# Kernel tuning notes

Hardware: AMD Instinct MI355X
Metric: run time of the kernel (lower is better)

## Reference

```python
import jax, jax.numpy as jnp
import numpy as np

B_J0 = 0.01   # baseline threshold
DT = 1.0
BETA = 1.8    # adaptation strength
LENS = 0.5
SCALE = 6.0
HIGHT = 0.15
GAMMA = 0.5


def _gauss(x, mu, sigma):
    return jnp.exp(-(x - mu) ** 2 / (2.0 * sigma ** 2)) / jnp.sqrt(2.0 * jnp.pi) / sigma


@jax.custom_vjp
def spike_fn(x):
    return (x > 0).astype(x.dtype)


def _spike_fwd(x):
    return spike_fn(x), x


def _spike_bwd(x, g):
    # multi-gaussian surrogate gradient (config.gradient_type == 'MG')
    temp = (_gauss(x, 0.0, LENS) * (1.0 + HIGHT)
            - _gauss(x, LENS, SCALE * LENS) * HIGHT
            - _gauss(x, -LENS, SCALE * LENS) * HIGHT)
    return (g * temp * GAMMA,)


spike_fn.defvjp(_spike_fwd, _spike_bwd)


def setup_inputs() -> dict:
    key = jax.random.key(0)
    ks = jax.random.split(key, 20)
    Bt, T, I, H, O = 256, 250, 700, 128, 20
    f32 = jnp.float32
    return {
        'x': jax.random.uniform(ks[0], (Bt, T, I), dtype=f32),
        'mask': jnp.ones((2, H, H), dtype=f32),
        'w_ih1': (jax.random.normal(ks[1], (I, H), dtype=f32) / np.sqrt(I).astype(np.float32)),
        'b_ih1': jnp.zeros((H,), f32),
        'w_h1h1': (jax.random.normal(ks[2], (H, H), dtype=f32) / np.sqrt(H).astype(np.float32)),
        'b_h1h1': jnp.zeros((H,), f32),
        'w_h1h2': (jax.random.normal(ks[3], (H, H), dtype=f32) / np.sqrt(H).astype(np.float32)),
        'b_h1h2': jnp.zeros((H,), f32),
        'w_h2h2': (jax.random.normal(ks[4], (H, H), dtype=f32) / np.sqrt(H).astype(np.float32)),
        'b_h2h2': jnp.zeros((H,), f32),
        'w_h2o': (jax.random.normal(ks[5], (H, O), dtype=f32) / np.sqrt(H).astype(np.float32)),
        'b_h2o': jnp.zeros((O,), f32),
        'tau_adp_h1': 150.0 + 10.0 * jax.random.normal(ks[6], (H,), dtype=f32),
        'tau_adp_h2': 150.0 + 10.0 * jax.random.normal(ks[7], (H,), dtype=f32),
        'tau_m_h1': 20.0 + 5.0 * jax.random.normal(ks[8], (H,), dtype=f32),
        'tau_m_h2': 20.0 + 5.0 * jax.random.normal(ks[9], (H,), dtype=f32),
        'tau_m_o': 20.0 + 5.0 * jax.random.normal(ks[10], (O,), dtype=f32),
        'hid1_mem0': jax.random.uniform(ks[11], (Bt, H), dtype=f32),
        'hid2_mem0': jax.random.uniform(ks[12], (Bt, H), dtype=f32),
        'out_mem0': jax.random.uniform(ks[13], (Bt, O), dtype=f32),
    }


def _forward(x, mask, w_ih1, b_ih1, w_h1h1, b_h1h1, w_h1h2, b_h1h2,
             w_h2h2, b_h2h2, w_h2o, b_h2o, tau_adp_h1, tau_adp_h2,
             tau_m_h1, tau_m_h2, tau_m_o, hid1_mem0, hid2_mem0, out_mem0):
    Bt, T, _ = x.shape
    H = w_ih1.shape[1]
    O = w_h2o.shape[1]
    # dropout mask applied to recurrent weights (weights stored [in, out])
    w11 = w_h1h1 * mask[0]
    w22 = w_h2h2 * mask[1]
    a1 = jnp.exp(-DT / tau_m_h1)
    r1 = jnp.exp(-DT / tau_adp_h1)
    a2 = jnp.exp(-DT / tau_m_h2)
    r2 = jnp.exp(-DT / tau_adp_h2)
    ao = jnp.exp(-DT / tau_m_o)
    # precompute input projection for all timesteps: [T, B, H]
    xin = jnp.einsum('bti,ih->tbh', x, w_ih1) + b_ih1

    def step(carry, inps):
        h1m, h1s, h2m, h2s, om, b1, b2, acc, s1, s2 = carry
        xt, t = inps
        # layer 1 (adaptive LIF)
        i1 = xt + h1s @ w11 + b_h1h1
        b1 = r1 * b1 + (1.0 - r1) * h1s
        B1 = B_J0 + BETA * b1
        h1m = h1m * a1 + (1.0 - a1) * i1 - B1 * h1s * DT
        h1s = spike_fn(h1m - B1)
        s1 = s1 + h1s
        # layer 2 (adaptive LIF)
        i2 = h1s @ w_h1h2 + b_h1h2 + h2s @ w22 + b_h2h2
        b2 = r2 * b2 + (1.0 - r2) * h2s
        B2 = B_J0 + BETA * b2
        h2m = h2m * a2 + (1.0 - a2) * i2 - B2 * h2s * DT
        h2s = spike_fn(h2m - B2)
        s2 = s2 + h2s
        # leaky-integrator readout (no spike)
        io = h2s @ w_h2o + b_h2o
        om = om * ao + (1.0 - ao) * io
        acc = acc + jnp.where(t > 10, jax.nn.softmax(om, axis=-1), 0.0)
        return (h1m, h1s, h2m, h2s, om, b1, b2, acc, s1, s2), None

    zH = jnp.zeros((Bt, H), x.dtype)
    carry0 = (hid1_mem0, zH, hid2_mem0, zH, out_mem0,
              jnp.full((Bt, H), B_J0, x.dtype), jnp.full((Bt, H), B_J0, x.dtype),
              jnp.zeros((Bt, O), x.dtype), zH, zH)
    carry, _ = jax.lax.scan(step, carry0, (xin, jnp.arange(T)))
    output, s1, s2 = carry[7], carry[8], carry[9]
    A_norm = jnp.sum(jnp.abs(w11)) + jnp.sum(jnp.abs(w22))
    return output, s1 / T, s2 / T, A_norm


def reference(x, mask, w_ih1, b_ih1, w_h1h1, b_h1h1, w_h1h2, b_h1h2,
              w_h2h2, b_h2h2, w_h2o, b_h2o, tau_adp_h1, tau_adp_h2,
              tau_m_h1, tau_m_h2, tau_m_o, hid1_mem0, hid2_mem0, out_mem0):
    return _forward(x, mask, w_ih1, b_ih1, w_h1h1, b_h1h1, w_h1h2, b_h1h2,
                    w_h2h2, b_h2h2, w_h2o, b_h2o, tau_adp_h1, tau_adp_h2,
                    tau_m_h1, tau_m_h2, tau_m_o, hid1_mem0, hid2_mem0, out_mem0)
```

## Files before the change

### kernel.cpp

```cpp
#include <hip/hip_runtime.h>
#include <math.h>

#define TT 250
#define BT 256
#define HN 128
#define ON 20
#define KIN 700
#define NKT 22

#define XIN_OFF 0
#define WPKH_OFF 8192000
#define WPKL_OFF 8237056

typedef __attribute__((ext_vector_type(8))) short bf16x8;
typedef __attribute__((ext_vector_type(4))) float f32x4;

__device__ __forceinline__ unsigned short bf16rne(float f) {
    unsigned u = __float_as_uint(f);
    unsigned r = u + 0x7fffu + ((u >> 16) & 1u);
    return (unsigned short)(r >> 16);
}
__device__ __forceinline__ void hilo(float v, short& h, short& l) {
    unsigned short hh = bf16rne(v);
    float vh = __uint_as_float((unsigned)hh << 16);
    h = (short)hh;
    l = (short)bf16rne(v - vh);
}

__device__ __forceinline__ void gl_lds16(const void* g, void* l) {
    __builtin_amdgcn_global_load_lds(
        (const __attribute__((address_space(1))) unsigned int*)g,
        (__attribute__((address_space(3))) unsigned int*)l, 16, 0, 0);
}

__global__ __launch_bounds__(256) void packw(const float* __restrict__ w,
                                             unsigned short* __restrict__ ph,
                                             unsigned short* __restrict__ pl) {
    int i = blockIdx.x * 256 + threadIdx.x;
    int k = i >> 7, c = i & 127;
    float v = (k < KIN) ? w[k * HN + c] : 0.f;
    short h, l;
    hilo(v, h, l);
    int dst = (((k >> 5) * 8 + (c >> 4)) * 64 + (((k >> 3) & 3) * 16 + (c & 15))) * 8 + (k & 7);
    ph[dst] = (unsigned short)h;
    pl[dst] = (unsigned short)l;
}

__global__ __launch_bounds__(512, 2) void gemm_in(const float* __restrict__ x,
        const unsigned short* __restrict__ wph, const unsigned short* __restrict__ wpl,
        const float* __restrict__ bias1, const float* __restrict__ bias2,
        float* __restrict__ xin) {
    __shared__ __align__(16) unsigned char wbuf[2][16384];
    __shared__ __align__(16) unsigned char xbuf[2][16384];
    const int tid = threadIdx.x;
    const int w = tid >> 6, lane = tid & 63;
    const int q = lane >> 4, li = lane & 15;
    const long mbase = (long)blockIdx.x * 128;

    const int xrow1 = tid >> 3;
    const int xrow2 = xrow1 + 64;
    const int xcs1 = (tid & 7) ^ (xrow1 & 7);
    const int xcs2 = (tid & 7) ^ (xrow2 & 7);
    const int wbase = w * 1024;

    f32x4 acc[8];
#pragma unroll
    for (int nt = 0; nt < 8; nt++) acc[nt] = (f32x4){0.f, 0.f, 0.f, 0.f};

    auto stage = [&](int kt, int buf) {
        char* wb = (char*)wbuf[buf];
        char* xb = (char*)xbuf[buf];
        gl_lds16((const char*)wph + kt * 8192 + tid * 16, wb + wbase);
        gl_lds16((const char*)wpl + kt * 8192 + tid * 16, wb + 8192 + wbase);
        int c1 = xcs1, c2 = xcs2;
        if (kt == NKT - 1) {
            if (c1 == 7) c1 = 6;
            if (c2 == 7) c2 = 6;
        }
        gl_lds16((const char*)x + (mbase + xrow1) * (KIN * 4) + kt * 128 + c1 * 16,
                 xb + wbase);
        gl_lds16((const char*)x + (mbase + xrow2) * (KIN * 4) + kt * 128 + c2 * 16,
                 xb + 8192 + wbase);
    };

    stage(0, 0);
    __syncthreads();

    const int xaddr = (w * 16 + li) * 128 + ((q * 32) ^ ((li & 7) << 4));

    for (int kt = 0; kt < NKT; kt++) {
        if (kt + 1 < NKT) stage(kt + 1, (kt + 1) & 1);

        const char* xc = (const char*)xbuf[kt & 1];
        float av[8];
        *(float4*)&av[0] = *(const float4*)(xc + xaddr);
        *(float4*)&av[4] = *(const float4*)(xc + (xaddr ^ 16));

        bf16x8 ah, al;
#pragma unroll
        for (int j = 0; j < 8; j++) {
            short h, l;
            hilo(av[j], h, l);
            ah[j] = h; al[j] = l;
        }

        const bf16x8* cv = (const bf16x8*)&wbuf[kt & 1][0];
#pragma unroll
        for (int nt = 0; nt < 8; nt++) {
            bf16x8 bh = cv[nt * 64 + lane];
            bf16x8 bl = cv[512 + nt * 64 + lane];
            acc[nt] = __builtin_amdgcn_mfma_f32_16x16x32_bf16(ah, bh, acc[nt], 0, 0, 0);
            acc[nt] = __builtin_amdgcn_mfma_f32_16x16x32_bf16(al, bh, acc[nt], 0, 0, 0);
            acc[nt] = __builtin_amdgcn_mfma_f32_16x16x32_bf16(ah, bl, acc[nt], 0, 0, 0);
        }
        __syncthreads();
    }

    float b12[8];
#pragma unroll
    for (int nt = 0; nt < 8; nt++) {
        int c = nt * 16 + li;
        b12[nt] = bias1[c] + bias2[c];
    }
#pragma unroll
    for (int r = 0; r < 4; r++) {
        long m = mbase + w * 16 + q * 4 + r;
        int bq = (int)(((unsigned long long)m * 67109ull) >> 24);
        int tt = (int)m - bq * 250;
        float* dst = xin + ((size_t)tt * BT + bq) * HN;
#pragma unroll
        for (int nt = 0; nt < 8; nt++) dst[nt * 16 + li] = acc[nt][r] + b12[nt];
    }
}

__global__ __launch_bounds__(512, 2) void snn_scan(
    const float* __restrict__ xin, const float* __restrict__ mask,
    const float* __restrict__ w_h1h1, const float* __restrict__ w_h1h2,
    const float* __restrict__ b_h1h2, const float* __restrict__ w_h2h2,
    const float* __restrict__ b_h2h2, const float* __restrict__ w_h2o,
    const float* __restrict__ b_h2o, const float* __restrict__ tau_adp1,
    const float* __restrict__ tau_adp2, const float* __restrict__ taum1,
    const float* __restrict__ taum2, const float* __restrict__ taumo,
    const float* __restrict__ h1m0, const float* __restrict__ h2m0,
    const float* __restrict__ om0, float* __restrict__ out) {

    __shared__ __align__(16) unsigned short sA1[2 * 2048];
    __shared__ __align__(16) unsigned short sA2[2 * 2048];
    __shared__ __align__(16) unsigned short sloW[8 * 3 * 4 * 64 * 8];
    __shared__ __align__(16) unsigned short sloO[2 * 4 * 64 * 8];
    __shared__ float omb[2][16 * ON];
    __shared__ float red[8];

    const int tid = threadIdx.x;
    const int w = tid >> 6, lane = tid & 63;
    const int q = lane >> 4, li = lane & 15;
    const int col = w * 16 + li;
    const int r0 = blockIdx.x * 16;

    bf16x8 h11[4], h22[4], h12[4], hO[4];
    const int ocol = (w == 6) ? li : 16 + li;
    const bool oval = (w >= 6) && (ocol < ON);
    bf16x8* lo11w = (bf16x8*)sloW + w * 768;
    bf16x8* lo22w = lo11w + 256;
    bf16x8* lo12w = lo11w + 512;
    bf16x8* loOw  = (bf16x8*)sloO + ((w >= 6) ? (w - 6) * 256 : 0);
    float pn = 0.f;
#pragma unroll
    for (int kt = 0; kt < 4; kt++) {
        bf16x8 L11, L22, L12, LO;
#pragma unroll
        for (int j = 0; j < 8; j++) {
            const int k = kt * 32 + q * 8 + j;
            const int idx = k * HN + col;
            float v11 = w_h1h1[idx] * mask[idx];
            float v22 = w_h2h2[idx] * mask[HN * HN + idx];
            float v12 = w_h1h2[idx];
            pn += fabsf(v11) + fabsf(v22);
            short hh, ll;
            hilo(v11, hh, ll); h11[kt][j] = hh; L11[j] = ll;
            hilo(v22, hh, ll); h22[kt][j] = hh; L22[j] = ll;
            hilo(v12, hh, ll); h12[kt][j] = hh; L12[j] = ll;
            float vO = oval ? w_h2o[k * ON + ocol] : 0.f;
            hilo(vO, hh, ll); hO[kt][j] = hh; LO[j] = ll;
        }
        lo11w[kt * 64 + lane] = L11;
        lo22w[kt * 64 + lane] = L22;
        lo12w[kt * 64 + lane] = L12;
        if (w >= 6) loOw[kt * 64 + lane] = LO;
    }

    const float a1 = expf(-1.f / taum1[col]);
    const float r1 = expf(-1.f / tau_adp1[col]);
    const float a2 = expf(-1.f / taum2[col]);
    const float r2 = expf(-1.f / tau_adp2[col]);
    const float cc2 = b_h1h2[col] + b_h2h2[col];
    float h1m[4], h2m[4], b1[4], b2[4], c1[4], c2n[4];
    unsigned s1bits = 0, s2bits = 0;
#pragma unroll
    for (int r = 0; r < 4; r++) {
        h1m[r] = h1m0[(r0 + q * 4 + r) * HN + col];
        h2m[r] = h2m0[(r0 + q * 4 + r) * HN + col];
        b1[r] = 0.01f; b2[r] = 0.01f; c1[r] = 0.f; c2n[r] = 0.f;
    }
    const float ao = oval ? expf(-1.f / taumo[ocol]) : 0.f;
    const float bo = oval ? b_h2o[ocol] : 0.f;
    float om[4];
#pragma unroll
    for (int r = 0; r < 4; r++)
        om[r] = oval ? om0[(r0 + q * 4 + r) * ON + ocol] : 0.f;
    const int sm = lane >> 2, ob = (lane & 3) * 5;
    float accs[5] = {0.f, 0.f, 0.f, 0.f, 0.f};

    {
        unsigned* z1 = (unsigned*)sA1;
        unsigned* z2 = (unsigned*)sA2;
        z1[tid] = 0u; z1[tid + 512] = 0u; z1[tid + 1024] = 0u; z1[tid + 1536] = 0u;
        z2[tid] = 0u; z2[tid + 512] = 0u; z2[tid + 1024] = 0u; z2[tid + 1536] = 0u;
    }

#pragma unroll
    for (int off = 32; off > 0; off >>= 1) pn += __shfl_down(pn, off);
    if (lane == 0) red[w] = pn;
    __syncthreads();
    if (tid == 0 && blockIdx.x == 0) {
        float s = 0.f;
#pragma unroll
        for (int i = 0; i < 8; i++) s += red[i];
        out[70656] = s;
    }

    const int wbase = (w >> 1) * 512 + (((2 * w + (li >> 3)) & 3) * 16 + q * 4) * 8 + (li & 7);
    const unsigned short ONE = 0x3F80u;

    const bf16x8* lo11r = (const bf16x8*)sloW + w * 768;
    const bf16x8* lo22r = lo11r + 256;
    const bf16x8* lo12r = lo11r + 512;
    const bf16x8* loOr  = (const bf16x8*)sloO + ((w >= 6) ? (w - 6) * 256 : 0);

    const float* xp = xin + (size_t)(r0 + q * 4) * HN + col;

    for (int i = 0; i < TT; i++) {
        const int pa = i & 1;

        float xt[4];
#pragma unroll
        for (int r = 0; r < 4; r++) xt[r] = xp[r * HN];
        xp += BT * HN;

        const bf16x8* g1p = (const bf16x8*)(sA1 + ((pa ^ 1) << 11));
        const bf16x8* f2p = (const bf16x8*)(sA2 + (pa << 11));
        bf16x8 g1[4], f2[4];
#pragma unroll
        for (int kt = 0; kt < 4; kt++) {
            g1[kt] = g1p[kt * 64 + lane];
            f2[kt] = f2p[kt * 64 + lane];
        }

        f32x4 aJ = {0.f, 0.f, 0.f, 0.f}, aG = {0.f, 0.f, 0.f, 0.f};
        {
            bf16x8 t12[4], t22[4];
#pragma unroll
            for (int kt = 0; kt < 4; kt++) {
                t12[kt] = lo12r[kt * 64 + lane];
                t22[kt] = lo22r[kt * 64 + lane];
            }
#pragma unroll
            for (int kt = 0; kt < 4; kt++) {
                aJ = __builtin_amdgcn_mfma_f32_16x16x32_bf16(g1[kt], h12[kt], aJ, 0, 0, 0);
                aJ = __builtin_amdgcn_mfma_f32_16x16x32_bf16(g1[kt], t12[kt], aJ, 0, 0, 0);
                aG = __builtin_amdgcn_mfma_f32_16x16x32_bf16(f2[kt], h22[kt], aG, 0, 0, 0);
                aG = __builtin_amdgcn_mfma_f32_16x16x32_bf16(f2[kt], t22[kt], aG, 0, 0, 0);
            }
        }
        f32x4 aO = {0.f, 0.f, 0.f, 0.f};
        if (w >= 6) {
            bf16x8 tO[4];
#pragma unroll
            for (int kt = 0; kt < 4; kt++) tO[kt] = loOr[kt * 64 + lane];
#pragma unroll
            for (int kt = 0; kt < 4; kt++) {
                aO = __builtin_amdgcn_mfma_f32_16x16x32_bf16(f2[kt], hO[kt], aO, 0, 0, 0);
                aO = __builtin_amdgcn_mfma_f32_16x16x32_bf16(f2[kt], tO[kt], aO, 0, 0, 0);
            }
        }
        f32x4 aI = {0.f, 0.f, 0.f, 0.f};
        {
            bf16x8 t11[4];
#pragma unroll
            for (int kt = 0; kt < 4; kt++) t11[kt] = lo11r[kt * 64 + lane];
#pragma unroll
            for (int kt = 0; kt < 4; kt++) {
                aI = __builtin_amdgcn_mfma_f32_16x16x32_bf16(g1[kt], h11[kt], aI, 0, 0, 0);
                aI = __builtin_amdgcn_mfma_f32_16x16x32_bf16(g1[kt], t11[kt], aI, 0, 0, 0);
            }
        }

        if (i >= 1) {
            unsigned short* s2w = sA2 + ((pa ^ 1) << 11);
#pragma unroll
            for (int r = 0; r < 4; r++) {
                const float sv = (float)((s2bits >> r) & 1u);
                const float i2 = aJ[r] + aG[r] + cc2;
                b2[r] = r2 * b2[r] + (1.f - r2) * sv;
                const float B = 0.01f + 1.8f * b2[r];
                h2m[r] = a2 * h2m[r] + (1.f - a2) * i2 - B * sv;
                const bool sp = (h2m[r] - B) > 0.f;
                s2bits = sp ? (s2bits | (1u << r)) : (s2bits & ~(1u << r));
                c2n[r] += sp ? 1.f : 0.f;
                s2w[wbase + r * 8] = sp ? ONE : (unsigned short)0;
            }
        }

        if (w >= 6 && i >= 2) {
#pragma unroll
            for (int r = 0; r < 4; r++) {
                om[r] = ao * om[r] + (1.f - ao) * (bo + aO[r]);
                if (oval) omb[pa][(q * 4 + r) * ON + ocol] = om[r];
            }
        }

        if (w == 0 && i >= 14) {
            float v[5], e[5];
            float mx = -1e30f;
#pragma unroll
            for (int s = 0; s < 5; s++) { v[s] = omb[pa ^ 1][sm * ON + ob + s]; mx = fmaxf(mx, v[s]); }
            mx = fmaxf(mx, __shfl_xor(mx, 1));
            mx = fmaxf(mx, __shfl_xor(mx, 2));
            float se = 0.f;
#pragma unroll
            for (int s = 0; s < 5; s++) { e[s] = __expf(v[s] - mx); se += e[s]; }
            se += __shfl_xor(se, 1);
            se += __shfl_xor(se, 2);
            const float inv = 1.f / se;
#pragma unroll
            for (int s = 0; s < 5; s++) accs[s] += e[s] * inv;
        }

        {
            unsigned short* s1w = sA1 + (pa << 11);
#pragma unroll
            for (int r = 0; r < 4; r++) {
                const float sv = (float)((s1bits >> r) & 1u);
                const float i1 = xt[r] + aI[r];
                b1[r] = r1 * b1[r] + (1.f - r1) * sv;
                const float B = 0.01f + 1.8f * b1[r];
                h1m[r] = a1 * h1m[r] + (1.f - a1) * i1 - B * sv;
                const bool sp = (h1m[r] - B) > 0.f;
                s1bits = sp ? (s1bits | (1u << r)) : (s1bits & ~(1u << r));
                c1[r] += sp ? 1.f : 0.f;
                s1w[wbase + r * 8] = sp ? ONE : (unsigned short)0;
            }
        }
        __syncthreads();
    }

    {
        const bf16x8* g1p = (const bf16x8*)(sA1 + 2048);
        const bf16x8* f2p = (const bf16x8*)(sA2);
        bf16x8 g1[4], f2[4], t12[4], t22[4];
#pragma unroll
        for (int kt = 0; kt < 4; kt++) {
            g1[kt] = g1p[kt * 64 + lane];
            f2[kt] = f2p[kt * 64 + lane];
            t12[kt] = lo12r[kt * 64 + lane];
            t22[kt] = lo22r[kt * 64 + lane];
        }
        f32x4 aJ = {0.f, 0.f, 0.f, 0.f}, aG = {0.f, 0.f, 0.f, 0.f};
#pragma unroll
        for (int kt = 0; kt < 4; kt++) {
            aJ = __builtin_amdgcn_mfma_f32_16x16x32_bf16(g1[kt], h12[kt], aJ, 0, 0, 0);
            aJ = __builtin_amdgcn_mfma_f32_16x16x32_bf16(g1[kt], t12[kt], aJ, 0, 0, 0);
            aG = __builtin_amdgcn_mfma_f32_16x16x32_bf16(f2[kt], h22[kt], aG, 0, 0, 0);
            aG = __builtin_amdgcn_mfma_f32_16x16x32_bf16(f2[kt], t22[kt], aG, 0, 0, 0);
        }
        f32x4 aO = {0.f, 0.f, 0.f, 0.f};
        if (w >= 6) {
            bf16x8 tO[4];
#pragma unroll
            for (int kt = 0; kt < 4; kt++) tO[kt] = loOr[kt * 64 + lane];
#pragma unroll
            for (int kt = 0; kt < 4; kt++) {
                aO = __builtin_amdgcn_mfma_f32_16x16x32_bf16(f2[kt], hO[kt], aO, 0, 0, 0);
                aO = __builtin_amdgcn_mfma_f32_16x16x32_bf16(f2[kt], tO[kt], aO, 0, 0, 0);
            }
        }
        {
            unsigned short* s2w = sA2 + 2048;
#pragma unroll
            for (int r = 0; r < 4; r++) {
                const float sv = (float)((s2bits >> r) & 1u);
                const float i2 = aJ[r] + aG[r] + cc2;
                b2[r] = r2 * b2[r] + (1.f - r2) * sv;
                const float B = 0.01f + 1.8f * b2[r];
                h2m[r] = a2 * h2m[r] + (1.f - a2) * i2 - B * sv;
                const bool sp = (h2m[r] - B) > 0.f;
                s2bits = sp ? (s2bits | (1u << r)) : (s2bits & ~(1u << r));
                c2n[r] += sp ? 1.f : 0.f;
                s2w[wbase + r * 8] = sp ? ONE : (unsigned short)0;
            }
        }
        if (w >= 6) {
#pragma unroll
            for (int r = 0; r < 4; r++) {
                om[r] = ao * om[r] + (1.f - ao) * (bo + aO[r]);
                if (oval) omb[0][(q * 4 + r) * ON + ocol] = om[r];
            }
        }
        if (w == 0) {
            float v[5], e[5];
            float mx = -1e30f;
#pragma unroll
            for (int s = 0; s < 5; s++) { v[s] = omb[1][sm * ON + ob + s]; mx = fmaxf(mx, v[s]); }
            mx = fmaxf(mx, __shfl_xor(mx, 1));
            mx = fmaxf(mx, __shfl_xor(mx, 2));
            float se = 0.f;
#pragma unroll
            for (int s = 0; s < 5; s++) { e[s] = __expf(v[s] - mx); se += e[s]; }
            se += __shfl_xor(se, 1);
            se += __shfl_xor(se, 2);
            const float inv = 1.f / se;
#pragma unroll
            for (int s = 0; s < 5; s++) accs[s] += e[s] * inv;
        }
        __syncthreads();
    }
    {
        if (w >= 6) {
            const bf16x8* f2p = (const bf16x8*)(sA2 + 2048);
            bf16x8 f2[4], tO[4];
#pragma unroll
            for (int kt = 0; kt < 4; kt++) {
                f2[kt] = f2p[kt * 64 + lane];
                tO[kt] = loOr[kt * 64 + lane];
            }
            f32x4 aO = {0.f, 0.f, 0.f, 0.f};
#pragma unroll
            for (int kt = 0; kt < 4; kt++) {
                aO = __builtin_amdgcn_mfma_f32_16x16x32_bf16(f2[kt], hO[kt], aO, 0, 0, 0);
                aO = __builtin_amdgcn_mfma_f32_16x16x32_bf16(f2[kt], tO[kt], aO, 0, 0, 0);
            }
#pragma unroll
            for (int r = 0; r < 4; r++) {
                om[r] = ao * om[r] + (1.f - ao) * (bo + aO[r]);
                if (oval) omb[1][(q * 4 + r) * ON + ocol] = om[r];
            }
        }
        if (w == 0) {
            float v[5], e[5];
            float mx = -1e30f;
#pragma unroll
            for (int s = 0; s < 5; s++) { v[s] = omb[0][sm * ON + ob + s]; mx = fmaxf(mx, v[s]); }
            mx = fmaxf(mx, __shfl_xor(mx, 1));
            mx = fmaxf(mx, __shfl_xor(mx, 2));
            float se = 0.f;
#pragma unroll
            for (int s = 0; s < 5; s++) { e[s] = __expf(v[s] - mx); se += e[s]; }
            se += __shfl_xor(se, 1);
            se += __shfl_xor(se, 2);
            const float inv = 1.f / se;
#pragma unroll
            for (int s = 0; s < 5; s++) accs[s] += e[s] * inv;
        }
        __syncthreads();
    }
    if (w == 0) {
        float v[5], e[5];
        float mx = -1e30f;
#pragma unroll
        for (int s = 0; s < 5; s++) { v[s] = omb[1][sm * ON + ob + s]; mx = fmaxf(mx, v[s]); }
        mx = fmaxf(mx, __shfl_xor(mx, 1));
        mx = fmaxf(mx, __shfl_xor(mx, 2));
        float se = 0.f;
#pragma unroll
        for (int s = 0; s < 5; s++) { e[s] = __expf(v[s] - mx); se += e[s]; }
        se += __shfl_xor(se, 1);
        se += __shfl_xor(se, 2);
        const float inv = 1.f / se;
#pragma unroll
        for (int s = 0; s < 5; s++) out[(r0 + sm) * ON + ob + s] = accs[s] + e[s] * inv;
    }
#pragma unroll
    for (int r = 0; r < 4; r++) {
        out[5120 + (r0 + q * 4 + r) * HN + col] = c1[r] * (1.f / 250.f);
        out[37888 + (r0 + q * 4 + r) * HN + col] = c2n[r] * (1.f / 250.f);
    }
}

extern "C" void kernel_launch(void* const* d_in, const int* in_sizes, int n_in,
                              void* d_out, int out_size, void* d_ws, size_t ws_size,
                              hipStream_t stream) {
    const float* x        = (const float*)d_in[0];
    const float* mask     = (const float*)d_in[1];
    const float* w_ih1    = (const float*)d_in[2];
    const float* b_ih1    = (const float*)d_in[3];
    const float* w_h1h1   = (const float*)d_in[4];
    const float* b_h1h1   = (const float*)d_in[5];
    const float* w_h1h2   = (const float*)d_in[6];
    const float* b_h1h2   = (const float*)d_in[7];
    const float* w_h2h2   = (const float*)d_in[8];
    const float* b_h2h2   = (const float*)d_in[9];
    const float* w_h2o    = (const float*)d_in[10];
    const float* b_h2o    = (const float*)d_in[11];
    const float* tau_adp1 = (const float*)d_in[12];
    const float* tau_adp2 = (const float*)d_in[13];
    const float* taum1    = (const float*)d_in[14];
    const float* taum2    = (const float*)d_in[15];
    const float* taumo    = (const float*)d_in[16];
    const float* h1m0     = (const float*)d_in[17];
    const float* h2m0     = (const float*)d_in[18];
    const float* om0      = (const float*)d_in[19];
    float* out = (float*)d_out;
    float* ws  = (float*)d_ws;

    float* xin = ws + XIN_OFF;
    unsigned short* wph = (unsigned short*)(ws + WPKH_OFF);
    unsigned short* wpl = (unsigned short*)(ws + WPKL_OFF);

    packw<<<352, 256, 0, stream>>>(w_ih1, wph, wpl);
    gemm_in<<<500, 512, 0, stream>>>(x, wph, wpl, b_ih1, b_h1h1, xin);
    snn_scan<<<16, 512, 0, stream>>>(xin, mask, w_h1h1, w_h1h2, b_h1h2, w_h2h2,
                                     b_h2h2, w_h2o, b_h2o, tau_adp1, tau_adp2,
                                     taum1, taum2, taumo, h1m0, h2m0, om0, out);
}
```

Before: 577.6 us.

## Keep low-part recurrent weights in registers and unroll scan by two

Moves the bf16 low-part weight fragments from LDS into registers and relaxes launch bounds to one block per CU so the extra VGPRs fit. The time loop is unrolled by two with ping-pong x prefetch registers, the MFMA block runs at raised priority, and the barrier becomes a raw LDS waitcnt plus s_barrier. This removes per-step LDS reads of weights and gives more overlap of the next x load. In exchange it lowers occupancy, and the lighter barrier relies on LDS-only synchronisation being sufficient.

```diff
diff --git a/kernel.cpp b/kernel.cpp
--- a/kernel.cpp
+++ b/kernel.cpp
@@ -26,6 +26,10 @@
     h = (short)hh;
     l = (short)bf16rne(v - vh);
 }
+
+#define LBAR() do { asm volatile("s_waitcnt lgkmcnt(0)" ::: "memory"); \
+                    __builtin_amdgcn_s_barrier();                      \
+                    asm volatile("" ::: "memory"); } while (0)
 
 __device__ __forceinline__ void gl_lds16(const void* g, void* l) {
     __builtin_amdgcn_global_load_lds(
@@ -133,7 +137,7 @@
     }
 }
 
-__global__ __launch_bounds__(512, 2) void snn_scan(
+__global__ __launch_bounds__(512, 1) void snn_scan(
     const float* __restrict__ xin, const float* __restrict__ mask,
     const float* __restrict__ w_h1h1, const float* __restrict__ w_h1h2,
     const float* __restrict__ b_h1h2, const float* __restrict__ w_h2h2,
@@ -146,8 +150,6 @@
 
     __shared__ __align__(16) unsigned short sA1[2 * 2048];
     __shared__ __align__(16) unsigned short sA2[2 * 2048];
-    __shared__ __align__(16) unsigned short sloW[8 * 3 * 4 * 64 * 8];
-    __shared__ __align__(16) unsigned short sloO[2 * 4 * 64 * 8];
     __shared__ float omb[2][16 * ON];
     __shared__ float red[8];
 
@@ -157,17 +159,12 @@
     const int col = w * 16 + li;
     const int r0 = blockIdx.x * 16;
 
-    bf16x8 h11[4], h22[4], h12[4], hO[4];
+    bf16x8 h11[4], l11[4], h22[4], l22[4], h12[4], l12[4], hO[4], lO[4];
     const int ocol = (w == 6) ? li : 16 + li;
     const bool oval = (w >= 6) && (ocol < ON);
-    bf16x8* lo11w = (bf16x8*)sloW + w * 768;
-    bf16x8* lo22w = lo11w + 256;
-    bf16x8* lo12w = lo11w + 512;
-    bf16x8* loOw  = (bf16x8*)sloO + ((w >= 6) ? (w - 6) * 256 : 0);
     float pn = 0.f;
 #pragma unroll
     for (int kt = 0; kt < 4; kt++) {
-        bf16x8 L11, L22, L12, LO;
 #pragma unroll
         for (int j = 0; j < 8; j++) {
             const int k = kt * 32 + q * 8 + j;
@@ -177,16 +174,12 @@
             float v12 = w_h1h2[idx];
             pn += fabsf(v11) + fabsf(v22);
             short hh, ll;
-            hilo(v11, hh, ll); h11[kt][j] = hh; L11[j] = ll;
-            hilo(v22, hh, ll); h22[kt][j] = hh; L22[j] = ll;
-            hilo(v12, hh, ll); h12[kt][j] = hh; L12[j] = ll;
+            hilo(v11, hh, ll); h11[kt][j] = hh; l11[kt][j] = ll;
+            hilo(v22, hh, ll); h22[kt][j] = hh; l22[kt][j] = ll;
+            hilo(v12, hh, ll); h12[kt][j] = hh; l12[kt][j] = ll;
             float vO = oval ? w_h2o[k * ON + ocol] : 0.f;
-            hilo(vO, hh, ll); hO[kt][j] = hh; LO[j] = ll;
-        }
-        lo11w[kt * 64 + lane] = L11;
-        lo22w[kt * 64 + lane] = L22;
-        lo12w[kt * 64 + lane] = L12;
-        if (w >= 6) loOw[kt * 64 + lane] = LO;
+            hilo(vO, hh, ll); hO[kt][j] = hh; lO[kt][j] = ll;
+        }
     }
 
     const float a1 = expf(-1.f / taum1[col]);
@@ -232,71 +225,135 @@
     const int wbase = (w >> 1) * 512 + (((2 * w + (li >> 3)) & 3) * 16 + q * 4) * 8 + (li & 7);
     const unsigned short ONE = 0x3F80u;
 
-    const bf16x8* lo11r = (const bf16x8*)sloW + w * 768;
-    const bf16x8* lo22r = lo11r + 256;
-    const bf16x8* lo12r = lo11r + 512;
-    const bf16x8* loOr  = (const bf16x8*)sloO + ((w >= 6) ? (w - 6) * 256 : 0);
-
     const float* xp = xin + (size_t)(r0 + q * 4) * HN + col;
-
-    for (int i = 0; i < TT; i++) {
-        const int pa = i & 1;
-
-        float xt[4];
-#pragma unroll
-        for (int r = 0; r < 4; r++) xt[r] = xp[r * HN];
-        xp += BT * HN;
-
-        const bf16x8* g1p = (const bf16x8*)(sA1 + ((pa ^ 1) << 11));
-        const bf16x8* f2p = (const bf16x8*)(sA2 + (pa << 11));
+    float xtA[4], xtB[4];
+    xtA[0] = xp[0]; xtA[1] = xp[HN]; xtA[2] = xp[2 * HN]; xtA[3] = xp[3 * HN];
+    xp += BT * HN;
+
+#define STEPX(PA, XTC, XTP, IV)                                                   \
+    {                                                                             \
+        const int i_ = (IV);                                                      \
+                       \
+        XTP[0] = xp[0]; XTP[1] = xp[HN]; XTP[2] = xp[2 * HN]; XTP[3] = xp[3 * HN];\
+        xp += BT * HN;                                                            \
+        const bf16x8* g1p_ = (const bf16x8*)(sA1 + (((PA) ^ 1) << 11));           \
+        const bf16x8* f2p_ = (const bf16x8*)(sA2 + ((PA) << 11));                 \
+        bf16x8 g1[4], f2[4];                                                      \
+        _Pragma("unroll")                                                         \
+        for (int kt = 0; kt < 4; kt++) {                                          \
+            g1[kt] = g1p_[kt * 64 + lane];                                        \
+            f2[kt] = f2p_[kt * 64 + lane];                                        \
+        }                                                                         \
+        f32x4 aI = {0.f, 0.f, 0.f, 0.f}, aJ = {0.f, 0.f, 0.f, 0.f},              \
+              aG = {0.f, 0.f, 0.f, 0.f};                                          \
+        __builtin_amdgcn_s_setprio(1);                                            \
+        _Pragma("unroll")                                                         \
+        for (int kt = 0; kt < 4; kt++) {                                          \
+            aI = __builtin_amdgcn_mfma_f32_16x16x32_bf16(g1[kt], h11[kt], aI, 0, 0, 0); \
+            aI = __builtin_amdgcn_mfma_f32_16x16x32_bf16(g1[kt], l11[kt], aI, 0, 0, 0); \
+            aJ = __builtin_amdgcn_mfma_f32_16x16x32_bf16(g1[kt], h12[kt], aJ, 0, 0, 0); \
+            aJ = __builtin_amdgcn_mfma_f32_16x16x32_bf16(g1[kt], l12[kt], aJ, 0, 0, 0); \
+            aG = __builtin_amdgcn_mfma_f32_16x16x32_bf16(f2[kt], h22[kt], aG, 0, 0, 0); \
+            aG = __builtin_amdgcn_mfma_f32_16x16x32_bf16(f2[kt], l22[kt], aG, 0, 0, 0); \
+        }                                                                         \
+        f32x4 aO = {0.f, 0.f, 0.f, 0.f};                                          \
+        if (w >= 6) {                                                             \
+            _Pragma("unroll")                                                     \
+            for (int kt = 0; kt < 4; kt++) {                                      \
+                aO = __builtin_amdgcn_mfma_f32_16x16x32_bf16(f2[kt], hO[kt], aO, 0, 0, 0); \
+                aO = __builtin_amdgcn_mfma_f32_16x16x32_bf16(f2[kt], lO[kt], aO, 0, 0, 0); \
+            }                                                                     \
+        }                                                                         \
+        __builtin_amdgcn_s_setprio(0);                                            \
+        if (i_ >= 1) {                                                            \
+            unsigned short* s2w = sA2 + (((PA) ^ 1) << 11);                       \
+            _Pragma("unroll")                                                     \
+            for (int r = 0; r < 4; r++) {                                         \
+                const float sv = (float)((s2bits >> r) & 1u);                     \
+                const float i2 = aJ[r] + aG[r] + cc2;                             \
+                b2[r] = r2 * b2[r] + (1.f - r2) * sv;                             \
+                const float B = 0.01f + 1.8f * b2[r];                             \
+                h2m[r] = a2 * h2m[r] + (1.f - a2) * i2 - B * sv;                  \
+                const bool sp = (h2m[r] - B) > 0.f;                               \
+                s2bits = sp ? (s2bits | (1u << r)) : (s2bits & ~(1u << r));       \
+                c2n[r] += sp ? 1.f : 0.f;                                         \
+                s2w[wbase + r * 8] = sp ? ONE : (unsigned short)0;                \
+            }                                                                     \
+        }                                                                         \
+        if (w >= 6 && i_ >= 2) {                                                  \
+            _Pragma("unroll")                                                     \
+            for (int r = 0; r < 4; r++) {                                         \
+                om[r] = ao * om[r] + (1.f - ao) * (bo + aO[r]);                   \
+                if (oval) omb[(PA)][(q * 4 + r) * ON + ocol] = om[r];             \
+            }                                                                     \
+        }                                                                         \
+        if (w == 0 && i_ >= 14) {                                                 \
+            float v_[5], e_[5];                                                   \
+            float mx = -1e30f;                                                    \
+            _Pragma("unroll")                                                     \
+            for (int s = 0; s < 5; s++) { v_[s] = omb[(PA) ^ 1][sm * ON + ob + s]; mx = fmaxf(mx, v_[s]); } \
+            mx = fmaxf(mx, __shfl_xor(mx, 1));                                    \
+            mx = fmaxf(mx, __shfl_xor(mx, 2));                                    \
+            float se = 0.f;                                                       \
+            _Pragma("unroll")                                                     \
+            for (int s = 0; s < 5; s++) { e_[s] = __expf(v_[s] - mx); se += e_[s]; } \
+            se += __shfl_xor(se, 1);                                              \
+            se += __shfl_xor(se, 2);                                              \
+            const float inv = 1.f / se;                                           \
+            _Pragma("unroll")                                                     \
+            for (int s = 0; s < 5; s++) accs[s] += e_[s] * inv;                   \
+        }                                                                         \
+        {                                                                         \
+            unsigned short* s1w = sA1 + ((PA) << 11);                             \
+            _Pragma("unroll")                                                     \
+            for (int r = 0; r < 4; r++) {                                         \
+                const float sv = (float)((s1bits >> r) & 1u);                     \
+                const float i1 = XTC[r] + aI[r];                                  \
+                b1[r] = r1 * b1[r] + (1.f - r1) * sv;                             \
+                const float B = 0.01f + 1.8f * b1[r];                             \
+                h1m[r] = a1 * h1m[r] + (1.f - a1) * i1 - B * sv;                  \
+                const bool sp = (h1m[r] - B) > 0.f;                               \
+                s1bits = sp ? (s1bits | (1u << r)) : (s1bits & ~(1u << r));       \
+                c1[r] += sp ? 1.f : 0.f;                                          \
+                s1w[wbase + r * 8] = sp ? ONE : (unsigned short)0;                \
+            }                                                                     \
+        }                                                                         \
+        LBAR();                                                                   \
+    }
+
+    for (int it = 0; it < TT; it += 2) {
+        STEPX(0, xtA, xtB, it);
+        STEPX(1, xtB, xtA, it + 1);
+    }
+#undef STEPX
+
+    {
+        const bf16x8* g1p = (const bf16x8*)(sA1 + 2048);
+        const bf16x8* f2p = (const bf16x8*)(sA2);
         bf16x8 g1[4], f2[4];
 #pragma unroll
         for (int kt = 0; kt < 4; kt++) {
             g1[kt] = g1p[kt * 64 + lane];
             f2[kt] = f2p[kt * 64 + lane];
         }
-
         f32x4 aJ = {0.f, 0.f, 0.f, 0.f}, aG = {0.f, 0.f, 0.f, 0.f};
-        {
-            bf16x8 t12[4], t22[4];
-#pragma unroll
-            for (int kt = 0; kt < 4; kt++) {
-                t12[kt] = lo12r[kt * 64 + lane];
-                t22[kt] = lo22r[kt * 64 + lane];
-            }
-#pragma unroll
-            for (int kt = 0; kt < 4; kt++) {
-                aJ = __builtin_amdgcn_mfma_f32_16x16x32_bf16(g1[kt], h12[kt], aJ, 0, 0, 0);
-                aJ = __builtin_amdgcn_mfma_f32_16x16x32_bf16(g1[kt], t12[kt], aJ, 0, 0, 0);
-                aG = __builtin_amdgcn_mfma_f32_16x16x32_bf16(f2[kt], h22[kt], aG, 0, 0, 0);
-                aG = __builtin_amdgcn_mfma_f32_16x16x32_bf16(f2[kt], t22[kt], aG, 0, 0, 0);
-            }
+#pragma unroll
+        for (int kt = 0; kt < 4; kt++) {
+            aJ = __builtin_amdgcn_mfma_f32_16x16x32_bf16(g1[kt], h12[kt], aJ, 0, 0, 0);
+            aJ = __builtin_amdgcn_mfma_f32_16x16x32_bf16(g1[kt], l12[kt], aJ, 0, 0, 0);
+            aG = __builtin_amdgcn_mfma_f32_16x16x32_bf16(f2[kt], h22[kt], aG, 0, 0, 0);
+            aG = __builtin_amdgcn_mfma_f32_16x16x32_bf16(f2[kt], l22[kt], aG, 0, 0, 0);
         }
         f32x4 aO = {0.f, 0.f, 0.f, 0.f};
         if (w >= 6) {
-            bf16x8 tO[4];
-#pragma unroll
-            for (int kt = 0; kt < 4; kt++) tO[kt] = loOr[kt * 64 + lane];
 #pragma unroll
             for (int kt = 0; kt < 4; kt++) {
                 aO = __builtin_amdgcn_mfma_f32_16x16x32_bf16(f2[kt], hO[kt], aO, 0, 0, 0);
-                aO = __builtin_amdgcn_mfma_f32_16x16x32_bf16(f2[kt], tO[kt], aO, 0, 0, 0);
+                aO = __builtin_amdgcn_mfma_f32_16x16x32_bf16(f2[kt], lO[kt], aO, 0, 0, 0);
             }
         }
-        f32x4 aI = {0.f, 0.f, 0.f, 0.f};
         {
-            bf16x8 t11[4];
-#pragma unroll
-            for (int kt = 0; kt < 4; kt++) t11[kt] = lo11r[kt * 64 + lane];
-#pragma unroll
-            for (int kt = 0; kt < 4; kt++) {
-                aI = __builtin_amdgcn_mfma_f32_16x16x32_bf16(g1[kt], h11[kt], aI, 0, 0, 0);
-                aI = __builtin_amdgcn_mfma_f32_16x16x32_bf16(g1[kt], t11[kt], aI, 0, 0, 0);
-            }
-        }
-
-        if (i >= 1) {
-            unsigned short* s2w = sA2 + ((pa ^ 1) << 11);
+            unsigned short* s2w = sA2 + 2048;
 #pragma unroll
             for (int r = 0; r < 4; r++) {
                 const float sv = (float)((s2bits >> r) & 1u);
@@ -310,20 +367,18 @@
                 s2w[wbase + r * 8] = sp ? ONE : (unsigned short)0;
             }
         }
-
-        if (w >= 6 && i >= 2) {
+        if (w >= 6) {
 #pragma unroll
             for (int r = 0; r < 4; r++) {
                 om[r] = ao * om[r] + (1.f - ao) * (bo + aO[r]);
-                if (oval) omb[pa][(q * 4 + r) * ON + ocol] = om[r];
+                if (oval) omb[0][(q * 4 + r) * ON + ocol] = om[r];
             }
         }
-
-        if (w == 0 && i >= 14) {
+        if (w == 0) {
             float v[5], e[5];
             float mx = -1e30f;
 #pragma unroll
-            for (int s = 0; s < 5; s++) { v[s] = omb[pa ^ 1][sm * ON + ob + s]; mx = fmaxf(mx, v[s]); }
+            for (int s = 0; s < 5; s++) { v[s] = omb[1][sm * ON + ob + s]; mx = fmaxf(mx, v[s]); }
             mx = fmaxf(mx, __shfl_xor(mx, 1));
             mx = fmaxf(mx, __shfl_xor(mx, 2));
             float se = 0.f;
@@ -335,109 +390,19 @@
 #pragma unroll
             for (int s = 0; s < 5; s++) accs[s] += e[s] * inv;
         }
-
-        {
-            unsigned short* s1w = sA1 + (pa << 11);
-#pragma unroll
-            for (int r = 0; r < 4; r++) {
-                const float sv = (float)((s1bits >> r) & 1u);
-                const float i1 = xt[r] + aI[r];
-                b1[r] = r1 * b1[r] + (1.f - r1) * sv;
-                const float B = 0.01f + 1.8f * b1[r];
-                h1m[r] = a1 * h1m[r] + (1.f - a1) * i1 - B * sv;
-                const bool sp = (h1m[r] - B) > 0.f;
-                s1bits = sp ? (s1bits | (1u << r)) : (s1bits & ~(1u << r));
-                c1[r] += sp ? 1.f : 0.f;
-                s1w[wbase + r * 8] = sp ? ONE : (unsigned short)0;
-            }
-        }
-        __syncthreads();
-    }
-
-    {
-        const bf16x8* g1p = (const bf16x8*)(sA1 + 2048);
-        const bf16x8* f2p = (const bf16x8*)(sA2);
-        bf16x8 g1[4], f2[4], t12[4], t22[4];
-#pragma unroll
-        for (int kt = 0; kt < 4; kt++) {
-            g1[kt] = g1p[kt * 64 + lane];
-            f2[kt] = f2p[kt * 64 + lane];
-            t12[kt] = lo12r[kt * 64 + lane];
-            t22[kt] = lo22r[kt * 64 + lane];
-        }
-        f32x4 aJ = {0.f, 0.f, 0.f, 0.f}, aG = {0.f, 0.f, 0.f, 0.f};
-#pragma unroll
-        for (int kt = 0; kt < 4; kt++) {
-            aJ = __builtin_amdgcn_mfma_f32_16x16x32_bf16(g1[kt], h12[kt], aJ, 0, 0, 0);
-            aJ = __builtin_amdgcn_mfma_f32_16x16x32_bf16(g1[kt], t12[kt], aJ, 0, 0, 0);
-            aG = __builtin_amdgcn_mfma_f32_16x16x32_bf16(f2[kt], h22[kt], aG, 0, 0, 0);
-            aG = __builtin_amdgcn_mfma_f32_16x16x32_bf16(f2[kt], t22[kt], aG, 0, 0, 0);
-        }
-        f32x4 aO = {0.f, 0.f, 0.f, 0.f};
-        if (w >= 6) {
-            bf16x8 tO[4];
-#pragma unroll
-            for (int kt = 0; kt < 4; kt++) tO[kt] = loOr[kt * 64 + lane];
-#pragma unroll
-            for (int kt = 0; kt < 4; kt++) {
-                aO = __builtin_amdgcn_mfma_f32_16x16x32_bf16(f2[kt], hO[kt], aO, 0, 0, 0);
-                aO = __builtin_amdgcn_mfma_f32_16x16x32_bf16(f2[kt], tO[kt], aO, 0, 0, 0);
-            }
-        }
-        {
-            unsigned short* s2w = sA2 + 2048;
-#pragma unroll
-            for (int r = 0; r < 4; r++) {
-                const float sv = (float)((s2bits >> r) & 1u);
-                const float i2 = aJ[r] + aG[r] + cc2;
-                b2[r] = r2 * b2[r] + (1.f - r2) * sv;
-                const float B = 0.01f + 1.8f * b2[r];
-                h2m[r] = a2 * h2m[r] + (1.f - a2) * i2 - B * sv;
-                const bool sp = (h2m[r] - B) > 0.f;
-                s2bits = sp ? (s2bits | (1u << r)) : (s2bits & ~(1u << r));
-                c2n[r] += sp ? 1.f : 0.f;
-                s2w[wbase + r * 8] = sp ? ONE : (unsigned short)0;
-            }
-        }
-        if (w >= 6) {
-#pragma unroll
-            for (int r = 0; r < 4; r++) {
-                om[r] = ao * om[r] + (1.f - ao) * (bo + aO[r]);
-                if (oval) omb[0][(q * 4 + r) * ON + ocol] = om[r];
-            }
-        }
-        if (w == 0) {
-            float v[5], e[5];
-            float mx = -1e30f;
-#pragma unroll
-            for (int s = 0; s < 5; s++) { v[s] = omb[1][sm * ON + ob + s]; mx = fmaxf(mx, v[s]); }
-            mx = fmaxf(mx, __shfl_xor(mx, 1));
-            mx = fmaxf(mx, __shfl_xor(mx, 2));
-            float se = 0.f;
-#pragma unroll
-            for (int s = 0; s < 5; s++) { e[s] = __expf(v[s] - mx); se += e[s]; }
-            se += __shfl_xor(se, 1);
-            se += __shfl_xor(se, 2);
-            const float inv = 1.f / se;
-#pragma unroll
-            for (int s = 0; s < 5; s++) accs[s] += e[s] * inv;
-        }
         __syncthreads();
     }
     {
         if (w >= 6) {
             const bf16x8* f2p = (const bf16x8*)(sA2 + 2048);
-            bf16x8 f2[4], tO[4];
-#pragma unroll
-            for (int kt = 0; kt < 4; kt++) {
-                f2[kt] = f2p[kt * 64 + lane];
-                tO[kt] = loOr[kt * 64 + lane];
-            }
+            bf16x8 f2[4];
+#pragma unroll
+            for (int kt = 0; kt < 4; kt++) f2[kt] = f2p[kt * 64 + lane];
             f32x4 aO = {0.f, 0.f, 0.f, 0.f};
 #pragma unroll
             for (int kt = 0; kt < 4; kt++) {
                 aO = __builtin_amdgcn_mfma_f32_16x16x32_bf16(f2[kt], hO[kt], aO, 0, 0, 0);
-                aO = __builtin_amdgcn_mfma_f32_16x16x32_bf16(f2[kt], tO[kt], aO, 0, 0, 0);
+                aO = __builtin_amdgcn_mfma_f32_16x16x32_bf16(f2[kt], lO[kt], aO, 0, 0, 0);
             }
 #pragma unroll
             for (int r = 0; r < 4; r++) {
```

Result: slower. 614.9 us (+6.5%).

## Keep split-bf16 recurrent weights in registers and split readout GEMM across warps

Applied to the files above, without the earlier changes.

The low-order bf16 halves of the recurrent weight matrices now live in registers instead of being reloaded from shared memory every timestep. This removes per-step LDS traffic and frees the large shared buffers. The output projection's hi and lo MFMA halves are split between warps 4-5 (lo part) and warps 6-7 (hi part). The lo partials are exchanged through a small shared buffer, which adds one more pipeline stage and an extra epilogue step. The cost is much higher VGPR pressure under launch_bounds(512,2), which risks spills or lower occupancy.

```diff
diff --git a/kernel.cpp b/kernel.cpp
--- a/kernel.cpp
+++ b/kernel.cpp
@@ -146,8 +146,7 @@
 
     __shared__ __align__(16) unsigned short sA1[2 * 2048];
     __shared__ __align__(16) unsigned short sA2[2 * 2048];
-    __shared__ __align__(16) unsigned short sloW[8 * 3 * 4 * 64 * 8];
-    __shared__ __align__(16) unsigned short sloO[2 * 4 * 64 * 8];
+    __shared__ __align__(16) float oxb[2][512];
     __shared__ float omb[2][16 * ON];
     __shared__ float red[8];
 
@@ -157,17 +156,13 @@
     const int col = w * 16 + li;
     const int r0 = blockIdx.x * 16;
 
-    bf16x8 h11[4], h22[4], h12[4], hO[4];
-    const int ocol = (w == 6) ? li : 16 + li;
-    const bool oval = (w >= 6) && (ocol < ON);
-    bf16x8* lo11w = (bf16x8*)sloW + w * 768;
-    bf16x8* lo22w = lo11w + 256;
-    bf16x8* lo12w = lo11w + 512;
-    bf16x8* loOw  = (bf16x8*)sloO + ((w >= 6) ? (w - 6) * 256 : 0);
+    bf16x8 h11[4], l11[4], h22[4], l22[4], h12[4], l12[4], wO[4];
+    const int ocol = ((w & 1) ? 16 : 0) + li;
+    const bool ow    = (w >= 4) && (ocol < ON);
+    const bool oval6 = (w >= 6) && (ocol < ON);
     float pn = 0.f;
 #pragma unroll
     for (int kt = 0; kt < 4; kt++) {
-        bf16x8 L11, L22, L12, LO;
 #pragma unroll
         for (int j = 0; j < 8; j++) {
             const int k = kt * 32 + q * 8 + j;
@@ -177,16 +172,13 @@
             float v12 = w_h1h2[idx];
             pn += fabsf(v11) + fabsf(v22);
             short hh, ll;
-            hilo(v11, hh, ll); h11[kt][j] = hh; L11[j] = ll;
-            hilo(v22, hh, ll); h22[kt][j] = hh; L22[j] = ll;
-            hilo(v12, hh, ll); h12[kt][j] = hh; L12[j] = ll;
-            float vO = oval ? w_h2o[k * ON + ocol] : 0.f;
-            hilo(vO, hh, ll); hO[kt][j] = hh; LO[j] = ll;
-        }
-        lo11w[kt * 64 + lane] = L11;
-        lo22w[kt * 64 + lane] = L22;
-        lo12w[kt * 64 + lane] = L12;
-        if (w >= 6) loOw[kt * 64 + lane] = LO;
+            hilo(v11, hh, ll); h11[kt][j] = hh; l11[kt][j] = ll;
+            hilo(v22, hh, ll); h22[kt][j] = hh; l22[kt][j] = ll;
+            hilo(v12, hh, ll); h12[kt][j] = hh; l12[kt][j] = ll;
+            float vO = ow ? w_h2o[k * ON + ocol] : 0.f;
+            hilo(vO, hh, ll);
+            wO[kt][j] = (w >= 6) ? hh : ll;
+        }
     }
 
     const float a1 = expf(-1.f / taum1[col]);
@@ -202,14 +194,17 @@
         h2m[r] = h2m0[(r0 + q * 4 + r) * HN + col];
         b1[r] = 0.01f; b2[r] = 0.01f; c1[r] = 0.f; c2n[r] = 0.f;
     }
-    const float ao = oval ? expf(-1.f / taumo[ocol]) : 0.f;
-    const float bo = oval ? b_h2o[ocol] : 0.f;
+    const float ao = oval6 ? expf(-1.f / taumo[ocol]) : 0.f;
+    const float bo = oval6 ? b_h2o[ocol] : 0.f;
     float om[4];
 #pragma unroll
     for (int r = 0; r < 4; r++)
-        om[r] = oval ? om0[(r0 + q * 4 + r) * ON + ocol] : 0.f;
+        om[r] = oval6 ? om0[(r0 + q * 4 + r) * ON + ocol] : 0.f;
     const int sm = lane >> 2, ob = (lane & 3) * 5;
     float accs[5] = {0.f, 0.f, 0.f, 0.f, 0.f};
+
+    f32x4 aOp = {0.f, 0.f, 0.f, 0.f};
+    const int oidx = ((w & 1) << 8) + lane * 4;
 
     {
         unsigned* z1 = (unsigned*)sA1;
@@ -232,11 +227,6 @@
     const int wbase = (w >> 1) * 512 + (((2 * w + (li >> 3)) & 3) * 16 + q * 4) * 8 + (li & 7);
     const unsigned short ONE = 0x3F80u;
 
-    const bf16x8* lo11r = (const bf16x8*)sloW + w * 768;
-    const bf16x8* lo22r = lo11r + 256;
-    const bf16x8* lo12r = lo11r + 512;
-    const bf16x8* loOr  = (const bf16x8*)sloO + ((w >= 6) ? (w - 6) * 256 : 0);
-
     const float* xp = xin + (size_t)(r0 + q * 4) * HN + col;
 
     for (int i = 0; i < TT; i++) {
@@ -256,43 +246,21 @@
             f2[kt] = f2p[kt * 64 + lane];
         }
 
-        f32x4 aJ = {0.f, 0.f, 0.f, 0.f}, aG = {0.f, 0.f, 0.f, 0.f};
-        {
-            bf16x8 t12[4], t22[4];
-#pragma unroll
-            for (int kt = 0; kt < 4; kt++) {
-                t12[kt] = lo12r[kt * 64 + lane];
-                t22[kt] = lo22r[kt * 64 + lane];
-            }
-#pragma unroll
-            for (int kt = 0; kt < 4; kt++) {
-                aJ = __builtin_amdgcn_mfma_f32_16x16x32_bf16(g1[kt], h12[kt], aJ, 0, 0, 0);
-                aJ = __builtin_amdgcn_mfma_f32_16x16x32_bf16(g1[kt], t12[kt], aJ, 0, 0, 0);
-                aG = __builtin_amdgcn_mfma_f32_16x16x32_bf16(f2[kt], h22[kt], aG, 0, 0, 0);
-                aG = __builtin_amdgcn_mfma_f32_16x16x32_bf16(f2[kt], t22[kt], aG, 0, 0, 0);
-            }
+        f32x4 aI = {0.f, 0.f, 0.f, 0.f}, aJ = {0.f, 0.f, 0.f, 0.f}, aG = {0.f, 0.f, 0.f, 0.f};
+#pragma unroll
+        for (int kt = 0; kt < 4; kt++) {
+            aI = __builtin_amdgcn_mfma_f32_16x16x32_bf16(g1[kt], h11[kt], aI, 0, 0, 0);
+            aI = __builtin_amdgcn_mfma_f32_16x16x32_bf16(g1[kt], l11[kt], aI, 0, 0, 0);
+            aJ = __builtin_amdgcn_mfma_f32_16x16x32_bf16(g1[kt], h12[kt], aJ, 0, 0, 0);
+            aJ = __builtin_amdgcn_mfma_f32_16x16x32_bf16(g1[kt], l12[kt], aJ, 0, 0, 0);
+            aG = __builtin_amdgcn_mfma_f32_16x16x32_bf16(f2[kt], h22[kt], aG, 0, 0, 0);
+            aG = __builtin_amdgcn_mfma_f32_16x16x32_bf16(f2[kt], l22[kt], aG, 0, 0, 0);
         }
         f32x4 aO = {0.f, 0.f, 0.f, 0.f};
-        if (w >= 6) {
-            bf16x8 tO[4];
-#pragma unroll
-            for (int kt = 0; kt < 4; kt++) tO[kt] = loOr[kt * 64 + lane];
-#pragma unroll
-            for (int kt = 0; kt < 4; kt++) {
-                aO = __builtin_amdgcn_mfma_f32_16x16x32_bf16(f2[kt], hO[kt], aO, 0, 0, 0);
-                aO = __builtin_amdgcn_mfma_f32_16x16x32_bf16(f2[kt], tO[kt], aO, 0, 0, 0);
-            }
-        }
-        f32x4 aI = {0.f, 0.f, 0.f, 0.f};
-        {
-            bf16x8 t11[4];
-#pragma unroll
-            for (int kt = 0; kt < 4; kt++) t11[kt] = lo11r[kt * 64 + lane];
-#pragma unroll
-            for (int kt = 0; kt < 4; kt++) {
-                aI = __builtin_amdgcn_mfma_f32_16x16x32_bf16(g1[kt], h11[kt], aI, 0, 0, 0);
-                aI = __builtin_amdgcn_mfma_f32_16x16x32_bf16(g1[kt], t11[kt], aI, 0, 0, 0);
-            }
+        if (w >= 4) {
+#pragma unroll
+            for (int kt = 0; kt < 4; kt++)
+                aO = __builtin_amdgcn_mfma_f32_16x16x32_bf16(f2[kt], wO[kt], aO, 0, 0, 0);
         }
 
         if (i >= 1) {
@@ -311,29 +279,35 @@
             }
         }
 
-        if (w >= 6 && i >= 2) {
-#pragma unroll
-            for (int r = 0; r < 4; r++) {
-                om[r] = ao * om[r] + (1.f - ao) * (bo + aO[r]);
-                if (oval) omb[pa][(q * 4 + r) * ON + ocol] = om[r];
-            }
-        }
-
-        if (w == 0 && i >= 14) {
-            float v[5], e[5];
+        if (w >= 4 && w < 6) {
+#pragma unroll
+            for (int r = 0; r < 4; r++) oxb[pa][oidx + r] = aO[r];
+        }
+
+        if (w >= 6 && i >= 3) {
+#pragma unroll
+            for (int r = 0; r < 4; r++) {
+                om[r] = ao * om[r] + (1.f - ao) * (bo + aOp[r] + oxb[pa ^ 1][oidx + r]);
+                if (oval6) omb[pa][(q * 4 + r) * ON + ocol] = om[r];
+            }
+        }
+        aOp = aO;
+
+        if (w == 0 && i >= 15) {
+            float v_[5], e_[5];
             float mx = -1e30f;
 #pragma unroll
-            for (int s = 0; s < 5; s++) { v[s] = omb[pa ^ 1][sm * ON + ob + s]; mx = fmaxf(mx, v[s]); }
+            for (int s = 0; s < 5; s++) { v_[s] = omb[pa ^ 1][sm * ON + ob + s]; mx = fmaxf(mx, v_[s]); }
             mx = fmaxf(mx, __shfl_xor(mx, 1));
             mx = fmaxf(mx, __shfl_xor(mx, 2));
             float se = 0.f;
 #pragma unroll
-            for (int s = 0; s < 5; s++) { e[s] = __expf(v[s] - mx); se += e[s]; }
+            for (int s = 0; s < 5; s++) { e_[s] = __expf(v_[s] - mx); se += e_[s]; }
             se += __shfl_xor(se, 1);
             se += __shfl_xor(se, 2);
             const float inv = 1.f / se;
 #pragma unroll
-            for (int s = 0; s < 5; s++) accs[s] += e[s] * inv;
+            for (int s = 0; s < 5; s++) accs[s] += e_[s] * inv;
         }
 
         {
@@ -357,32 +331,25 @@
     {
         const bf16x8* g1p = (const bf16x8*)(sA1 + 2048);
         const bf16x8* f2p = (const bf16x8*)(sA2);
-        bf16x8 g1[4], f2[4], t12[4], t22[4];
+        bf16x8 g1[4], f2[4];
 #pragma unroll
         for (int kt = 0; kt < 4; kt++) {
             g1[kt] = g1p[kt * 64 + lane];
             f2[kt] = f2p[kt * 64 + lane];
-            t12[kt] = lo12r[kt * 64 + lane];
-            t22[kt] = lo22r[kt * 64 + lane];
         }
         f32x4 aJ = {0.f, 0.f, 0.f, 0.f}, aG = {0.f, 0.f, 0.f, 0.f};
 #pragma unroll
         for (int kt = 0; kt < 4; kt++) {
             aJ = __builtin_amdgcn_mfma_f32_16x16x32_bf16(g1[kt], h12[kt], aJ, 0, 0, 0);
-            aJ = __builtin_amdgcn_mfma_f32_16x16x32_bf16(g1[kt], t12[kt], aJ, 0, 0, 0);
+            aJ = __builtin_amdgcn_mfma_f32_16x16x32_bf16(g1[kt], l12[kt], aJ, 0, 0, 0);
             aG = __builtin_amdgcn_mfma_f32_16x16x32_bf16(f2[kt], h22[kt], aG, 0, 0, 0);
-            aG = __builtin_amdgcn_mfma_f32_16x16x32_bf16(f2[kt], t22[kt], aG, 0, 0, 0);
+            aG = __builtin_amdgcn_mfma_f32_16x16x32_bf16(f2[kt], l22[kt], aG, 0, 0, 0);
         }
         f32x4 aO = {0.f, 0.f, 0.f, 0.f};
-        if (w >= 6) {
-            bf16x8 tO[4];
-#pragma unroll
-            for (int kt = 0; kt < 4; kt++) tO[kt] = loOr[kt * 64 + lane];
-#pragma unroll
-            for (int kt = 0; kt < 4; kt++) {
-                aO = __builtin_amdgcn_mfma_f32_16x16x32_bf16(f2[kt], hO[kt], aO, 0, 0, 0);
-                aO = __builtin_amdgcn_mfma_f32_16x16x32_bf16(f2[kt], tO[kt], aO, 0, 0, 0);
-            }
+        if (w >= 4) {
+#pragma unroll
+            for (int kt = 0; kt < 4; kt++)
+                aO = __builtin_amdgcn_mfma_f32_16x16x32_bf16(f2[kt], wO[kt], aO, 0, 0, 0);
         }
         {
             unsigned short* s2w = sA2 + 2048;
@@ -399,13 +366,18 @@
                 s2w[wbase + r * 8] = sp ? ONE : (unsigned short)0;
             }
         }
+        if (w >= 4 && w < 6) {
+#pragma unroll
+            for (int r = 0; r < 4; r++) oxb[0][oidx + r] = aO[r];
+        }
         if (w >= 6) {
 #pragma unroll
             for (int r = 0; r < 4; r++) {
-                om[r] = ao * om[r] + (1.f - ao) * (bo + aO[r]);
-                if (oval) omb[0][(q * 4 + r) * ON + ocol] = om[r];
-            }
-        }
+                om[r] = ao * om[r] + (1.f - ao) * (bo + aOp[r] + oxb[1][oidx + r]);
+                if (oval6) omb[0][(q * 4 + r) * ON + ocol] = om[r];
+            }
+        }
+        aOp = aO;
         if (w == 0) {
             float v[5], e[5];
             float mx = -1e30f;
@@ -425,26 +397,28 @@
         __syncthreads();
     }
     {
+        f32x4 aO = {0.f, 0.f, 0.f, 0.f};
+        if (w >= 4) {
+            const bf16x8* f2p = (const bf16x8*)(sA2 + 2048);
+            bf16x8 f2[4];
+#pragma unroll
+            for (int kt = 0; kt < 4; kt++) f2[kt] = f2p[kt * 64 + lane];
+#pragma unroll
+            for (int kt = 0; kt < 4; kt++)
+                aO = __builtin_amdgcn_mfma_f32_16x16x32_bf16(f2[kt], wO[kt], aO, 0, 0, 0);
+        }
+        if (w >= 4 && w < 6) {
+#pragma unroll
+            for (int r = 0; r < 4; r++) oxb[1][oidx + r] = aO[r];
+        }
         if (w >= 6) {
-            const bf16x8* f2p = (const bf16x8*)(sA2 + 2048);
-            bf16x8 f2[4], tO[4];
-#pragma unroll
-            for (int kt = 0; kt < 4; kt++) {
-                f2[kt] = f2p[kt * 64 + lane];
-                tO[kt] = loOr[kt * 64 + lane];
-            }
-            f32x4 aO = {0.f, 0.f, 0.f, 0.f};
-#pragma unroll
-            for (int kt = 0; kt < 4; kt++) {
-                aO = __builtin_amdgcn_mfma_f32_16x16x32_bf16(f2[kt], hO[kt], aO, 0, 0, 0);
-                aO = __builtin_amdgcn_mfma_f32_16x16x32_bf16(f2[kt], tO[kt], aO, 0, 0, 0);
-            }
-#pragma unroll
-            for (int r = 0; r < 4; r++) {
-                om[r] = ao * om[r] + (1.f - ao) * (bo + aO[r]);
-                if (oval) omb[1][(q * 4 + r) * ON + ocol] = om[r];
-            }
-        }
+#pragma unroll
+            for (int r = 0; r < 4; r++) {
+                om[r] = ao * om[r] + (1.f - ao) * (bo + aOp[r] + oxb[0][oidx + r]);
+                if (oval6) omb[1][(q * 4 + r) * ON + ocol] = om[r];
+            }
+        }
+        aOp = aO;
         if (w == 0) {
             float v[5], e[5];
             float mx = -1e30f;
@@ -463,11 +437,37 @@
         }
         __syncthreads();
     }
+    {
+        if (w >= 6) {
+#pragma unroll
+            for (int r = 0; r < 4; r++) {
+                om[r] = ao * om[r] + (1.f - ao) * (bo + aOp[r] + oxb[1][oidx + r]);
+                if (oval6) omb[0][(q * 4 + r) * ON + ocol] = om[r];
+            }
+        }
+        if (w == 0) {
+            float v[5], e[5];
+            float mx = -1e30f;
+#pragma unroll
+            for (int s = 0; s < 5; s++) { v[s] = omb[1][sm * ON + ob + s]; mx = fmaxf(mx, v[s]); }
+            mx = fmaxf(mx, __shfl_xor(mx, 1));
+            mx = fmaxf(mx, __shfl_xor(mx, 2));
+            float se = 0.f;
+#pragma unroll
+            for (int s = 0; s < 5; s++) { e[s] = __expf(v[s] - mx); se += e[s]; }
+            se += __shfl_xor(se, 1);
+            se += __shfl_xor(se, 2);
+            const float inv = 1.f / se;
+#pragma unroll
+            for (int s = 0; s < 5; s++) accs[s] += e[s] * inv;
+        }
+        __syncthreads();
+    }
     if (w == 0) {
         float v[5], e[5];
         float mx = -1e30f;
 #pragma unroll
-        for (int s = 0; s < 5; s++) { v[s] = omb[1][sm * ON + ob + s]; mx = fmaxf(mx, v[s]); }
+        for (int s = 0; s < 5; s++) { v[s] = omb[0][sm * ON + ob + s]; mx = fmaxf(mx, v[s]); }
         mx = fmaxf(mx, __shfl_xor(mx, 1));
         mx = fmaxf(mx, __shfl_xor(mx, 2));
         float se = 0.f;
```

Result: no change. 585.7 us (+1.4%).
